# Kernel tuning notes

Hardware: AMD Instinct MI355X
Metric: run time of the kernel (lower is better)

## Reference

```python
import jax, jax.numpy as jnp
import numpy as np

EMB_DIM = 512
NUM_HEADS = 8
HEAD_DIM = EMB_DIM // NUM_HEADS


def setup_inputs() -> dict:
    key = jax.random.key(0)
    ks = jax.random.split(key, 8)
    B, S, D = 2, 192, EMB_DIM
    return {
        "q": jax.random.normal(ks[0], (B, S, D), dtype=jnp.float32),
        "k": jax.random.normal(ks[1], (B, S, D), dtype=jnp.float32),
        "l": jax.random.normal(ks[2], (B, S, D), dtype=jnp.float32),
        "v": jax.random.normal(ks[3], (B, S, D), dtype=jnp.float32),
        "Wq": jax.random.normal(ks[4], (D, D), dtype=jnp.float32) * (1.0 / np.sqrt(D)),
        "Wk": jax.random.normal(ks[5], (D, D), dtype=jnp.float32) * (1.0 / np.sqrt(D)),
        "Wv": jax.random.normal(ks[6], (D, D), dtype=jnp.float32) * (1.0 / np.sqrt(D)),
        "Wout": jax.random.normal(ks[7], (D, D), dtype=jnp.float32) * (1.0 / np.sqrt(D)),
    }


def _heads(x, W):
    # torch nn.Linear: x @ W.T ; then split heads -> (B, H, S, hd)
    B, S, D = x.shape
    y = x @ W.T
    return y.reshape(B, S, NUM_HEADS, HEAD_DIM).transpose(0, 2, 1, 3)


def reference(q, k, l, v, Wq, Wk, Wv, Wout):
    B, QS, D = q.shape
    KS, LS = k.shape[1], l.shape[1]
    qh = _heads(q, Wq)
    kh = _heads(k, Wk)
    lh = _heads(l, Wk)  # NOTE: original module projects l with self.key (faithful)
    vh = _heads(v, Wv)
    # rank-3 attention scores: (B, H, QS, KS, LS)
    scores = jnp.einsum('bhqe,bhke,bhle->bhqkl', qh, kh, lh) / jnp.sqrt(
        jnp.asarray(HEAD_DIM, dtype=q.dtype))
    # softmax jointly over (KS, LS)
    attn = jax.nn.softmax(scores.reshape(B, NUM_HEADS, QS, KS * LS), axis=-1)
    attn = attn.reshape(B, NUM_HEADS, QS, KS, LS)
    # vv[b,h,l,k,d] = v[b,h,k,d]; contract over k and l -> (B, QS, H, hd)
    attended = jnp.einsum('bhqkl,bhkd->bqhd', attn, vh)
    concatenated = attended.reshape(B, QS, EMB_DIM)
    return concatenated @ Wout.T
```

## Files before the change

kernel.cpp:

```cpp
#include <hip/hip_runtime.h>
#include <math.h>

#define BB 2
#define SS 192
#define DD 512
#define HH 8
#define HD 64
#define QCB 6
#define NQC (SS / QCB)
#define PROJ_N (BB*HH*SS*HD)
#define SCL (0.125f * 1.44269504088896f)

typedef __attribute__((ext_vector_type(4))) float f32x4;
typedef _Float16 f16x8 __attribute__((ext_vector_type(8)));

__device__ __forceinline__ f16x8 cvt8_f16_rne(const float* g) {
    f16x8 r;
#pragma unroll
    for (int i = 0; i < 8; ++i) r[i] = (_Float16)g[i];
    return r;
}

template <int SPLIT>
__device__ __forceinline__ void gemm_mfma_body(const float* __restrict__ x,
                                               const float* __restrict__ W,
                                               float* __restrict__ y) {
    __shared__ short Ahs[2][4 * 64 * 8];
    __shared__ short Bhs[2][4 * 64 * 8];

    const int t = threadIdx.x;
    const int lane = t & 63, w = t >> 6;
    const int wr = w >> 1, wc = w & 1;
    const int c16 = lane & 15, q4 = lane >> 4;
    const int m0 = blockIdx.x * 64, n0 = blockIdx.y * 64;
    const int sr = t >> 2, scc = t & 3;

    f32x4 acc[2][2];
#pragma unroll
    for (int a = 0; a < 2; ++a)
#pragma unroll
        for (int b = 0; b < 2; ++b) acc[a][b] = (f32x4){0.f, 0.f, 0.f, 0.f};

#define STAGE(kk, bf)                                                              \
    {                                                                              \
        float a8[8], w8[8];                                                        \
        *(f32x4*)&a8[0] = *(const f32x4*)&x[(m0 + sr) * 512 + (kk) + scc * 8];     \
        *(f32x4*)&a8[4] = *(const f32x4*)&x[(m0 + sr) * 512 + (kk) + scc * 8 + 4]; \
        *(f32x4*)&w8[0] = *(const f32x4*)&W[(n0 + sr) * 512 + (kk) + scc * 8];     \
        *(f32x4*)&w8[4] = *(const f32x4*)&W[(n0 + sr) * 512 + (kk) + scc * 8 + 4]; \
        *(f16x8*)&Ahs[bf][(scc * 64 + sr) * 8] = cvt8_f16_rne(a8);                 \
        *(f16x8*)&Bhs[bf][(scc * 64 + sr) * 8] = cvt8_f16_rne(w8);                 \
    }

    STAGE(0, 0)
    for (int s = 0; s < 16; ++s) {
        __syncthreads();
        if (s + 1 < 16) STAGE((s + 1) * 32, (s + 1) & 1)
        const int b = s & 1;
        f16x8 aH[2], bH[2];
#pragma unroll
        for (int mt = 0; mt < 2; ++mt) {
            const int row = wr * 32 + mt * 16 + c16;
            aH[mt] = *(const f16x8*)&Ahs[b][(q4 * 64 + row) * 8];
        }
#pragma unroll
        for (int nt = 0; nt < 2; ++nt) {
            const int col = wc * 32 + nt * 16 + c16;
            bH[nt] = *(const f16x8*)&Bhs[b][(q4 * 64 + col) * 8];
        }
#pragma unroll
        for (int mt = 0; mt < 2; ++mt)
#pragma unroll
            for (int nt = 0; nt < 2; ++nt)
                acc[mt][nt] = __builtin_amdgcn_mfma_f32_16x16x32_f16(aH[mt], bH[nt], acc[mt][nt], 0, 0, 0);
    }
#undef STAGE

#pragma unroll
    for (int mt = 0; mt < 2; ++mt)
#pragma unroll
        for (int nt = 0; nt < 2; ++nt)
#pragma unroll
            for (int j = 0; j < 4; ++j) {
                const int n_row = m0 + wr * 32 + mt * 16 + q4 * 4 + j;
                const int col = n0 + wc * 32 + nt * 16 + c16;
                const float v = acc[mt][nt][j];
                if (SPLIT) {
                    const int b = n_row / SS, s2 = n_row % SS;
                    const int h = col >> 6, e = col & 63;
                    y[((b * HH + h) * SS + s2) * HD + e] = v;
                } else {
                    y[n_row * 512 + col] = v;
                }
            }
}

__global__ __launch_bounds__(256) void proj4_kernel(
    const float* __restrict__ xq, const float* __restrict__ xk,
    const float* __restrict__ xl, const float* __restrict__ xv,
    const float* __restrict__ Wq, const float* __restrict__ Wk,
    const float* __restrict__ Wv, float* __restrict__ ws) {
    const int p = blockIdx.z;
    const float* x = (p == 0) ? xq : (p == 1) ? xk : (p == 2) ? xl : xv;
    const float* W = (p == 0) ? Wq : (p == 3) ? Wv : Wk;
    gemm_mfma_body<1>(x, W, ws + p * PROJ_N);
}

__global__ __launch_bounds__(256) void outproj_kernel(
    const float* __restrict__ att, const float* __restrict__ Wout,
    float* __restrict__ out) {
    gemm_mfma_body<0>(att, Wout, out);
}

__global__ __launch_bounds__(512, 4) void attn3d_mfma_kernel(
    const float* __restrict__ qh, const float* __restrict__ kh,
    const float* __restrict__ lh, const float* __restrict__ vh,
    float* __restrict__ att) {
    __shared__ short Kf16[8][193][8];
    __shared__ short Lf16[8][193][8];
    __shared__ short qpk[QCB][8][8];
    __shared__ float partial[2][QCB][196];
    __shared__ float Wt[QCB][192];
    __shared__ float zinv[QCB];

    const int blk = blockIdx.x;
    const int bh = blk >> 5, qc = blk & 31;
    const int t = threadIdx.x;
    const int lane = t & 63, w = t >> 6;
    const int lg = w >> 2, kg = w & 3;
    const int c = lane & 15, eh = lane >> 4;

    if (t < QCB * 64) {
        const int q = t >> 6, e = t & 63;
        const float v = qh[(bh * SS + qc * QCB + q) * HD + e] * SCL;
        qpk[q][e >> 3][e & 7] = __builtin_bit_cast(short, (_Float16)v);
    }
#pragma unroll
    for (int j = 0; j < 3; ++j) {
        const int cid = t + 512 * j;
        const int k = cid >> 3, ec = cid & 7;
        float b8[8];
        const float* kp = &kh[(bh * SS + k) * HD + ec * 8];
        *(f32x4*)&b8[0] = *(const f32x4*)&kp[0];
        *(f32x4*)&b8[4] = *(const f32x4*)&kp[4];
        *(f16x8*)&Kf16[ec][k][0] = cvt8_f16_rne(b8);
        const float* lp = &lh[(bh * SS + k) * HD + ec * 8];
        *(f32x4*)&b8[0] = *(const f32x4*)&lp[0];
        *(f32x4*)&b8[4] = *(const f32x4*)&lp[4];
        *(f16x8*)&Lf16[ec][k][0] = cvt8_f16_rne(b8);
    }
    __syncthreads();

    for (int qi = 0; qi < QCB; ++qi) {
        const int q = (qi + w) % QCB;
        const f16x8 qf0 = *(const f16x8*)&qpk[q][eh][0];
        const f16x8 qf1 = *(const f16x8*)&qpk[q][4 + eh][0];
        f16x8 Bf[3][2];
#pragma unroll
        for (int kt = 0; kt < 3; ++kt) {
            const int col = kg * 48 + kt * 16 + c;
            Bf[kt][0] = *(const f16x8*)&Kf16[eh][col][0] * qf0;
            Bf[kt][1] = *(const f16x8*)&Kf16[4 + eh][col][0] * qf1;
        }
        float rr0 = 0.f, rr1 = 0.f, rr2 = 0.f;
#pragma unroll
        for (int lt = 0; lt < 6; ++lt) {
            const int row = lg * 96 + lt * 16 + c;
            const f16x8 A0 = *(const f16x8*)&Lf16[eh][row][0];
            const f16x8 A1 = *(const f16x8*)&Lf16[4 + eh][row][0];
            f32x4 a0 = (f32x4){0.f, 0.f, 0.f, 0.f};
            f32x4 a1 = (f32x4){0.f, 0.f, 0.f, 0.f};
            f32x4 a2 = (f32x4){0.f, 0.f, 0.f, 0.f};
            a0 = __builtin_amdgcn_mfma_f32_16x16x32_f16(A0, Bf[0][0], a0, 0, 0, 0);
            a1 = __builtin_amdgcn_mfma_f32_16x16x32_f16(A0, Bf[1][0], a1, 0, 0, 0);
            a2 = __builtin_amdgcn_mfma_f32_16x16x32_f16(A0, Bf[2][0], a2, 0, 0, 0);
            a0 = __builtin_amdgcn_mfma_f32_16x16x32_f16(A1, Bf[0][1], a0, 0, 0, 0);
            a1 = __builtin_amdgcn_mfma_f32_16x16x32_f16(A1, Bf[1][1], a1, 0, 0, 0);
            a2 = __builtin_amdgcn_mfma_f32_16x16x32_f16(A1, Bf[2][1], a2, 0, 0, 0);
            rr0 += (__builtin_amdgcn_exp2f(a0[0]) + __builtin_amdgcn_exp2f(a0[1])) +
                   (__builtin_amdgcn_exp2f(a0[2]) + __builtin_amdgcn_exp2f(a0[3]));
            rr1 += (__builtin_amdgcn_exp2f(a1[0]) + __builtin_amdgcn_exp2f(a1[1])) +
                   (__builtin_amdgcn_exp2f(a1[2]) + __builtin_amdgcn_exp2f(a1[3]));
            rr2 += (__builtin_amdgcn_exp2f(a2[0]) + __builtin_amdgcn_exp2f(a2[1])) +
                   (__builtin_amdgcn_exp2f(a2[2]) + __builtin_amdgcn_exp2f(a2[3]));
        }
        rr0 += __shfl_xor(rr0, 16, 64);
        rr1 += __shfl_xor(rr1, 16, 64);
        rr2 += __shfl_xor(rr2, 16, 64);
        rr0 += __shfl_xor(rr0, 32, 64);
        rr1 += __shfl_xor(rr1, 32, 64);
        rr2 += __shfl_xor(rr2, 32, 64);
        if (eh == 0) {
            partial[lg][q][kg * 48 + 0 * 16 + c] = rr0;
            partial[lg][q][kg * 48 + 1 * 16 + c] = rr1;
            partial[lg][q][kg * 48 + 2 * 16 + c] = rr2;
        }
    }
    __syncthreads();

    for (int id = t; id < QCB * 192; id += 512) {
        const int q = id / 192, k = id - q * 192;
        Wt[q][k] = partial[0][q][k] + partial[1][q][k];
    }
    __syncthreads();

    if (w < QCB) {
        const int q = w;
        float z = Wt[q][lane] + Wt[q][lane + 64] + Wt[q][lane + 128];
#pragma unroll
        for (int off = 32; off >= 1; off >>= 1) z += __shfl_xor(z, off, 64);
        if (lane == 0) zinv[q] = 1.f / z;
    }
    __syncthreads();

    const int b = bh >> 3, h = bh & 7;
    if (t < QCB * 64) {
        const int q = t >> 6, d = t & 63;
        const float* vp = vh + bh * SS * HD + d;
        float sum = 0.f;
        for (int k0 = 0; k0 < SS; k0 += 8) {
            float v8[8];
#pragma unroll
            for (int j = 0; j < 8; ++j) v8[j] = vp[(k0 + j) * HD];
#pragma unroll
            for (int j = 0; j < 8; ++j) sum = fmaf(Wt[q][k0 + j], v8[j], sum);
        }
        att[(b * SS + qc * QCB + q) * DD + h * HD + d] = sum * zinv[q];
    }
}

extern "C" void kernel_launch(void* const* d_in, const int* in_sizes, int n_in,
                              void* d_out, int out_size, void* d_ws, size_t ws_size,
                              hipStream_t stream) {
    (void)in_sizes; (void)n_in; (void)out_size; (void)ws_size;
    const float* q    = (const float*)d_in[0];
    const float* k    = (const float*)d_in[1];
    const float* l    = (const float*)d_in[2];
    const float* v    = (const float*)d_in[3];
    const float* Wq   = (const float*)d_in[4];
    const float* Wk   = (const float*)d_in[5];
    const float* Wv   = (const float*)d_in[6];
    const float* Wout = (const float*)d_in[7];
    float* out = (float*)d_out;

    float* ws  = (float*)d_ws;
    float* qhp = ws + 0 * PROJ_N;
    float* khp = ws + 1 * PROJ_N;
    float* lhp = ws + 2 * PROJ_N;
    float* vhp = ws + 3 * PROJ_N;
    float* atp = ws + 4 * PROJ_N;

    proj4_kernel<<<dim3(384 / 64, 512 / 64, 4), 256, 0, stream>>>(
        q, k, l, v, Wq, Wk, Wv, ws);
    attn3d_mfma_kernel<<<dim3(16 * NQC), 512, 0, stream>>>(qhp, khp, lhp, vhp, atp);
    outproj_kernel<<<dim3(384 / 64, 512 / 64), 256, 0, stream>>>(atp, Wout, out);
}
```

Baseline: 49.88 us.

## Fuse output projection into attention kernel and split-K projections with atomics

The output projection is folded into the attention kernel: each block multiplies its per-head attended rows by that head's slice of Wout with MFMA and atomically accumulates into the output. This removes the separate outproj launch and the global round-trip of the attended tensor. The input projections are split along K into two halves with atomicAdd to double the grid, and a zero kernel is added to clear the workspace and output first. The cost is an extra launch, atomic traffic, and partial-tile MFMA waste, since only 6 of 16 rows are used.

```diff
diff --git a/kernel.cpp b/kernel.cpp
--- a/kernel.cpp
+++ b/kernel.cpp
@@ -21,10 +21,25 @@
     return r;
 }
 
-template <int SPLIT>
-__device__ __forceinline__ void gemm_mfma_body(const float* __restrict__ x,
-                                               const float* __restrict__ W,
-                                               float* __restrict__ y) {
+__global__ __launch_bounds__(256) void zero_kernel(float* __restrict__ wsp,
+                                                   float* __restrict__ out) {
+    const int i = blockIdx.x * 256 + threadIdx.x;
+    if (i < 4 * PROJ_N) wsp[i] = 0.f;
+    if (i < BB * SS * DD) out[i] = 0.f;
+}
+
+__global__ __launch_bounds__(256) void proj4_kernel(
+    const float* __restrict__ xq, const float* __restrict__ xk,
+    const float* __restrict__ xl, const float* __restrict__ xv,
+    const float* __restrict__ Wq, const float* __restrict__ Wk,
+    const float* __restrict__ Wv, float* __restrict__ ws) {
+    const int z = blockIdx.z;
+    const int p = z >> 1;
+    const int k0 = (z & 1) * 256;
+    const float* x = (p == 0) ? xq : (p == 1) ? xk : (p == 2) ? xl : xv;
+    const float* W = (p == 0) ? Wq : (p == 3) ? Wv : Wk;
+    float* y = ws + p * PROJ_N;
+
     __shared__ short Ahs[2][4 * 64 * 8];
     __shared__ short Bhs[2][4 * 64 * 8];
 
@@ -52,10 +67,10 @@
         *(f16x8*)&Bhs[bf][(scc * 64 + sr) * 8] = cvt8_f16_rne(w8);                 \
     }
 
-    STAGE(0, 0)
-    for (int s = 0; s < 16; ++s) {
+    STAGE(k0, 0)
+    for (int s = 0; s < 8; ++s) {
         __syncthreads();
-        if (s + 1 < 16) STAGE((s + 1) * 32, (s + 1) & 1)
+        if (s + 1 < 8) STAGE(k0 + (s + 1) * 32, (s + 1) & 1)
         const int b = s & 1;
         f16x8 aH[2], bH[2];
 #pragma unroll
@@ -84,43 +99,22 @@
             for (int j = 0; j < 4; ++j) {
                 const int n_row = m0 + wr * 32 + mt * 16 + q4 * 4 + j;
                 const int col = n0 + wc * 32 + nt * 16 + c16;
-                const float v = acc[mt][nt][j];
-                if (SPLIT) {
-                    const int b = n_row / SS, s2 = n_row % SS;
-                    const int h = col >> 6, e = col & 63;
-                    y[((b * HH + h) * SS + s2) * HD + e] = v;
-                } else {
-                    y[n_row * 512 + col] = v;
-                }
+                const int b = n_row / SS, s2 = n_row % SS;
+                const int h = col >> 6, e = col & 63;
+                atomicAdd(&y[((b * HH + h) * SS + s2) * HD + e], acc[mt][nt][j]);
             }
-}
-
-__global__ __launch_bounds__(256) void proj4_kernel(
-    const float* __restrict__ xq, const float* __restrict__ xk,
-    const float* __restrict__ xl, const float* __restrict__ xv,
-    const float* __restrict__ Wq, const float* __restrict__ Wk,
-    const float* __restrict__ Wv, float* __restrict__ ws) {
-    const int p = blockIdx.z;
-    const float* x = (p == 0) ? xq : (p == 1) ? xk : (p == 2) ? xl : xv;
-    const float* W = (p == 0) ? Wq : (p == 3) ? Wv : Wk;
-    gemm_mfma_body<1>(x, W, ws + p * PROJ_N);
-}
-
-__global__ __launch_bounds__(256) void outproj_kernel(
-    const float* __restrict__ att, const float* __restrict__ Wout,
-    float* __restrict__ out) {
-    gemm_mfma_body<0>(att, Wout, out);
 }
 
 __global__ __launch_bounds__(512, 4) void attn3d_mfma_kernel(
     const float* __restrict__ qh, const float* __restrict__ kh,
     const float* __restrict__ lh, const float* __restrict__ vh,
-    float* __restrict__ att) {
+    const float* __restrict__ Wout, float* __restrict__ out) {
     __shared__ short Kf16[8][193][8];
     __shared__ short Lf16[8][193][8];
     __shared__ short qpk[QCB][8][8];
     __shared__ float partial[2][QCB][196];
     __shared__ float Wt[QCB][192];
+    __shared__ float attd[16][72];
     __shared__ float zinv[QCB];
 
     const int blk = blockIdx.x;
@@ -202,6 +196,7 @@
         const int q = id / 192, k = id - q * 192;
         Wt[q][k] = partial[0][q][k] + partial[1][q][k];
     }
+    for (int id = t; id < 16 * 72; id += 512) ((float*)attd)[id] = 0.f;
     __syncthreads();
 
     if (w < QCB) {
@@ -213,7 +208,6 @@
     }
     __syncthreads();
 
-    const int b = bh >> 3, h = bh & 7;
     if (t < QCB * 64) {
         const int q = t >> 6, d = t & 63;
         const float* vp = vh + bh * SS * HD + d;
@@ -225,7 +219,41 @@
 #pragma unroll
             for (int j = 0; j < 8; ++j) sum = fmaf(Wt[q][k0 + j], v8[j], sum);
         }
-        att[(b * SS + qc * QCB + q) * DD + h * HD + d] = sum * zinv[q];
+        attd[q][d] = sum * zinv[q];
+    }
+    __syncthreads();
+
+    const int b = bh >> 3, h = bh & 7;
+    f16x8 Ae0, Ae1;
+    {
+        float a8[8];
+        *(f32x4*)&a8[0] = *(const f32x4*)&attd[c][eh * 8];
+        *(f32x4*)&a8[4] = *(const f32x4*)&attd[c][eh * 8 + 4];
+        Ae0 = cvt8_f16_rne(a8);
+        *(f32x4*)&a8[0] = *(const f32x4*)&attd[c][32 + eh * 8];
+        *(f32x4*)&a8[4] = *(const f32x4*)&attd[c][32 + eh * 8 + 4];
+        Ae1 = cvt8_f16_rne(a8);
+    }
+#pragma unroll
+    for (int jt = 0; jt < 4; ++jt) {
+        const int j = (w * 4 + jt) * 16 + c;
+        const float* wp = &Wout[j * DD + h * HD];
+        float b8[8];
+        *(f32x4*)&b8[0] = *(const f32x4*)&wp[eh * 8];
+        *(f32x4*)&b8[4] = *(const f32x4*)&wp[eh * 8 + 4];
+        const f16x8 B0 = cvt8_f16_rne(b8);
+        *(f32x4*)&b8[0] = *(const f32x4*)&wp[32 + eh * 8];
+        *(f32x4*)&b8[4] = *(const f32x4*)&wp[32 + eh * 8 + 4];
+        const f16x8 B1 = cvt8_f16_rne(b8);
+        f32x4 oc = (f32x4){0.f, 0.f, 0.f, 0.f};
+        oc = __builtin_amdgcn_mfma_f32_16x16x32_f16(Ae0, B0, oc, 0, 0, 0);
+        oc = __builtin_amdgcn_mfma_f32_16x16x32_f16(Ae1, B1, oc, 0, 0, 0);
+#pragma unroll
+        for (int jj = 0; jj < 4; ++jj) {
+            const int q = eh * 4 + jj;
+            if (q < QCB)
+                atomicAdd(&out[(b * SS + qc * QCB + q) * DD + (w * 4 + jt) * 16 + c], oc[jj]);
+        }
     }
 }
 
@@ -248,10 +276,9 @@
     float* khp = ws + 1 * PROJ_N;
     float* lhp = ws + 2 * PROJ_N;
     float* vhp = ws + 3 * PROJ_N;
-    float* atp = ws + 4 * PROJ_N;
-
-    proj4_kernel<<<dim3(384 / 64, 512 / 64, 4), 256, 0, stream>>>(
+
+    zero_kernel<<<dim3((4 * PROJ_N + 255) / 256), 256, 0, stream>>>(ws, out);
+    proj4_kernel<<<dim3(384 / 64, 512 / 64, 8), 256, 0, stream>>>(
         q, k, l, v, Wq, Wk, Wv, ws);
-    attn3d_mfma_kernel<<<dim3(16 * NQC), 512, 0, stream>>>(qhp, khp, lhp, vhp, atp);
-    outproj_kernel<<<dim3(384 / 64, 512 / 64), 256, 0, stream>>>(atp, Wout, out);
-}
+    attn3d_mfma_kernel<<<dim3(16 * NQC), 512, 0, stream>>>(qhp, khp, lhp, vhp, Wout, out);
+}
```

Result: no change. 49.70 us (-0.4%).
